# Kernel tuning notes

Hardware: AMD Instinct MI355X
Metric: run time of the kernel (lower is better)

The kernel has to match this reference:

```python
import jax, jax.numpy as jnp
import numpy as np

H = 16          # num_heads
D = 1024        # in_features
NH = D // H     # per-head dim
EPS = 1e-5


def _ln(x, g, b):
    m = jnp.mean(x, axis=-1, keepdims=True)
    v = jnp.mean((x - m) ** 2, axis=-1, keepdims=True)
    return (x - m) / jnp.sqrt(v + EPS) * g + b


def _mha(q, k, v, Wq, bq, Wk, bk, Wv, bv, causal):
    # q: [Tq,B,D], k/v: [Tk,B,D]
    Tq, B, _ = q.shape
    Tk = k.shape[0]
    qh = (q @ Wq + bq).reshape(Tq, B, H, NH)
    kh = (k @ Wk + bk).reshape(Tk, B, H, NH)
    vh = (v @ Wv + bv).reshape(Tk, B, H, NH)
    scale = 1.0 / np.float32(np.sqrt(NH))
    logits = jnp.einsum('qbhd,kbhd->bhqk', qh, kh) * scale  # [B,H,Tq,Tk]
    if causal:
        mask = jnp.tril(jnp.ones((Tq, Tk), dtype=bool))
        logits = jnp.where(mask, logits, -jnp.inf)  # softmax over prefix [0..t]
    w = jax.nn.softmax(logits, axis=-1)
    out = jnp.einsum('bhqk,kbhd->qbhd', w, vh).reshape(Tq, B, D)
    return out


def setup_inputs() -> dict:
    key = jax.random.key(0)
    ks = jax.random.split(key, 12)
    s = 0.02
    T, B = 1024, 8
    inp = {
        'encoder_input': jax.random.normal(ks[0], (T, B, D), jnp.float32),
        'decoder_input': jax.random.normal(ks[1], (T, B, D), jnp.float32),
        # self-attention projections
        'Wq1': jax.random.normal(ks[2], (D, D), jnp.float32) * s,
        'bq1': jnp.zeros((D,), jnp.float32),
        'Wk1': jax.random.normal(ks[3], (D, D), jnp.float32) * s,
        'bk1': jnp.zeros((D,), jnp.float32),
        'Wv1': jax.random.normal(ks[4], (D, D), jnp.float32) * s,
        'bv1': jnp.zeros((D,), jnp.float32),
        # cross-attention projections
        'Wq2': jax.random.normal(ks[5], (D, D), jnp.float32) * s,
        'bq2': jnp.zeros((D,), jnp.float32),
        'Wk2': jax.random.normal(ks[6], (D, D), jnp.float32) * s,
        'bk2': jnp.zeros((D,), jnp.float32),
        'Wv2': jax.random.normal(ks[7], (D, D), jnp.float32) * s,
        'bv2': jnp.zeros((D,), jnp.float32),
        # position-wise linear
        'Wl': jax.random.normal(ks[8], (D, D), jnp.float32) * s,
        'bl': jnp.zeros((D,), jnp.float32),
        # layernorms
        'g1': jnp.ones((D,), jnp.float32), 'be1': jnp.zeros((D,), jnp.float32),
        'g2': jnp.ones((D,), jnp.float32), 'be2': jnp.zeros((D,), jnp.float32),
        'g3': jnp.ones((D,), jnp.float32), 'be3': jnp.zeros((D,), jnp.float32),
    }
    return inp


def reference(encoder_input, decoder_input,
              Wq1, bq1, Wk1, bk1, Wv1, bv1,
              Wq2, bq2, Wk2, bk2, Wv2, bv2,
              Wl, bl, g1, be1, g2, be2, g3, be3):
    # causal self-attention (prefix [:t+1] per step == causal mask)
    x = _mha(decoder_input, decoder_input, decoder_input,
             Wq1, bq1, Wk1, bk1, Wv1, bv1, causal=True)
    x = _ln(x + decoder_input, g1, be1)
    # cross-attention over full encoder input
    y = _mha(x, encoder_input, encoder_input,
             Wq2, bq2, Wk2, bk2, Wv2, bv2, causal=False)
    y = _ln(y + x, g2, be2)
    # position-wise linear (no activation in source) + residual + LN
    z = y @ Wl + bl
    out = _ln(z + y, g3, be3)
    return out
```

## Files before the change

kernel.cpp:

```cpp
#include <hip/hip_runtime.h>
#include <hip/hip_bf16.h>

typedef __bf16 bf16x8 __attribute__((ext_vector_type(8)));
typedef float f32x4 __attribute__((ext_vector_type(4)));

#define MFMA16(A, B, C) __builtin_amdgcn_mfma_f32_16x16x32_bf16(A, B, C, 0, 0, 0)

#define GLDS(gp, lp)                                                              \
    __builtin_amdgcn_global_load_lds(                                             \
        (const __attribute__((address_space(1))) void*)(gp),                      \
        (__attribute__((address_space(3))) void*)(lp), 16, 0, 0)

struct PtrW { const float* p[7]; };
__global__ __launch_bounds__(256) void wt_transpose(PtrW W, __hip_bfloat16* __restrict__ Wt) {
    const float* __restrict__ src = W.p[blockIdx.z];
    __hip_bfloat16* __restrict__ dst = Wt + ((size_t)blockIdx.z << 20);
    __shared__ float tile[32][33];
    const int bn = blockIdx.x * 32;
    const int bk = blockIdx.y * 32;
    const int tx = threadIdx.x, ty = threadIdx.y;
#pragma unroll
    for (int i = 0; i < 4; i++) {
        tile[ty + i * 8][tx] = src[(size_t)(bk + ty + i * 8) * 1024 + bn + tx];
    }
    __syncthreads();
#pragma unroll
    for (int i = 0; i < 4; i++) {
        dst[(size_t)(bn + ty + i * 8) * 1024 + bk + tx] =
            __float2bfloat16(tile[tx][ty + i * 8]);
    }
}

struct PtrC { const float* s[2]; __hip_bfloat16* d[2]; };
__global__ __launch_bounds__(256) void to_bf16(PtrC c) {
    const int z = blockIdx.y;
    const int i = (blockIdx.x * 256 + threadIdx.x) * 4;
    const float4 v = *(const float4*)(c.s[z] + i);
    __align__(8) __hip_bfloat16 t[4] = {__float2bfloat16(v.x), __float2bfloat16(v.y),
                                        __float2bfloat16(v.z), __float2bfloat16(v.w)};
    *(uint2*)(c.d[z] + i) = *(const uint2*)t;
}

struct Ptr5 { const float* p[5]; };
__global__ __launch_bounds__(256) void bias_concat(Ptr5 srcs, float* __restrict__ dst) {
    const int i = threadIdx.x * 4;
    *(float4*)(dst + blockIdx.x * 1024 + i) = *(const float4*)(srcs.p[blockIdx.x] + i);
}

__global__ __launch_bounds__(256) void v_transpose(const __hip_bfloat16* __restrict__ src,
                                                   __hip_bfloat16* __restrict__ Vt,
                                                   int S, int coloff) {
    __shared__ __hip_bfloat16 tile[64][72];
    const int t0 = blockIdx.x * 64;
    const int bh = blockIdx.y;
    const int b = bh & 7, h = bh >> 3;
    const int tid = threadIdx.x;
    const int r = tid >> 2, c = (tid & 3) * 16;
    const __hip_bfloat16* sp =
        src + (size_t)((t0 + r) * 8 + b) * S + coloff + h * 64 + c;
    *(uint4*)(&tile[r][c]) = *(const uint4*)(sp);
    *(uint4*)(&tile[r][c + 8]) = *(const uint4*)(sp + 8);
    __syncthreads();
    const int d = tid >> 2, tc = (tid & 3) * 16;
    __align__(16) __hip_bfloat16 tmp[16];
#pragma unroll
    for (int j = 0; j < 16; j++) tmp[j] = tile[tc + j][d];
    __hip_bfloat16* op = Vt + ((size_t)(b * 16 + h) << 16) + (size_t)d * 1024 + t0 + tc;
    *(uint4*)(op) = *(const uint4*)(tmp);
    *(uint4*)(op + 8) = *(const uint4*)(tmp + 8);
}

__global__ __launch_bounds__(256) void gemm_bias_kernel(
    const __hip_bfloat16* __restrict__ A, const __hip_bfloat16* __restrict__ Bt,
    const float* __restrict__ bias, float* __restrict__ Cf,
    __hip_bfloat16* __restrict__ Cb, int M, int N, int K,
    float qscale, int qcols) {
    __shared__ __align__(16) __hip_bfloat16 As[2][128 * 32];
    __shared__ __align__(16) __hip_bfloat16 Bs[2][128 * 32];
    const int tid = threadIdx.x;
    const int wave = tid >> 6, lane = tid & 63;
    const int quad = lane >> 4, l16 = lane & 15;
    const int m0 = blockIdx.x * 128, n0 = blockIdx.y * 128;
    const int wm = (wave & 1) * 64, wn = (wave >> 1) * 64;
    const int srow = lane >> 2;
    const int lc = (lane & 3) ^ ((lane >> 3) & 3);
    const __hip_bfloat16* ap[2];
    const __hip_bfloat16* bp[2];
    int loff[2];
#pragma unroll
    for (int u = 0; u < 2; u++) {
        const int g = wave * 2 + u;
        const int row = g * 16 + srow;
        ap[u] = A + (size_t)(m0 + row) * K + lc * 8;
        bp[u] = Bt + (size_t)(n0 + row) * K + lc * 8;
        loff[u] = g * 512;
    }
    const int pch = quad ^ ((l16 >> 1) & 3);
    f32x4 acc[4][4] = {};
#pragma unroll
    for (int u = 0; u < 2; u++) {
        GLDS(ap[u], &As[0][loff[u]]);
        GLDS(bp[u], &Bs[0][loff[u]]);
    }
    int sel = 0;
    for (int k0 = 0; k0 < K; k0 += 32) {
        __syncthreads();
        if (k0 + 32 < K) {
#pragma unroll
            for (int u = 0; u < 2; u++) {
                GLDS(ap[u] + k0 + 32, &As[sel ^ 1][loff[u]]);
                GLDS(bp[u] + k0 + 32, &Bs[sel ^ 1][loff[u]]);
            }
        }
        bf16x8 af[4], bfr[4];
#pragma unroll
        for (int i = 0; i < 4; i++) {
            af[i] = *(const bf16x8*)(&As[sel][(wm + i * 16 + l16) * 32 + pch * 8]);
            bfr[i] = *(const bf16x8*)(&Bs[sel][(wn + i * 16 + l16) * 32 + pch * 8]);
        }
#pragma unroll
        for (int i = 0; i < 4; i++)
#pragma unroll
            for (int j = 0; j < 4; j++)
                acc[i][j] = MFMA16(af[i], bfr[j], acc[i][j]);
        sel ^= 1;
    }
#pragma unroll
    for (int i = 0; i < 4; i++) {
#pragma unroll
        for (int j = 0; j < 4; j++) {
            const int mr = m0 + wm + i * 16 + quad * 4;
            const int nc = n0 + wn + j * 16 + l16;
            const float sc = (nc < qcols) ? qscale : 1.0f;
            const float bv = bias[nc];
#pragma unroll
            for (int r = 0; r < 4; r++) {
                const float v = (acc[i][j][r] + bv) * sc;
                const size_t idx = (size_t)(mr + r) * N + nc;
                if (Cf) Cf[idx] = v;
                if (Cb) Cb[idx] = __float2bfloat16(v);
            }
        }
    }
}

__global__ __launch_bounds__(256) void attn_kernel(
    const __hip_bfloat16* __restrict__ Qp, const __hip_bfloat16* __restrict__ Kp,
    const __hip_bfloat16* __restrict__ Vt, __hip_bfloat16* __restrict__ Ob,
    int T, int qRS, int kRS, int causal) {
    __shared__ __align__(16) __hip_bfloat16 Ks[2][64 * 64];
    __shared__ __align__(16) __hip_bfloat16 Vs[2][64 * 64];
    __shared__ __align__(16) __hip_bfloat16 Ps[4][16 * 64];
    const int tid = threadIdx.x, wave = tid >> 6, lane = tid & 63;
    const int quad = lane >> 4, l16 = lane & 15;
    const int gid = blockIdx.x;
    const int bh = (gid & 7) * 16 + (gid >> 7);
    const int qt = (gid >> 3) & 15;
    const int b = bh & 7, h = bh >> 3;
    const int q0 = qt * 64;
    const int qstride = 8 * qRS, kstride = 8 * kRS;
    const int sw = l16 & 7;

    const int myq = q0 + wave * 16 + l16;
    bf16x8 qf0, qf1;
    {
        const __hip_bfloat16* qptr = Qp + (size_t)b * qRS + h * 64 + (size_t)myq * qstride;
        qf0 = *(const bf16x8*)(qptr + quad * 8);
        qf1 = *(const bf16x8*)(qptr + 32 + quad * 8);
    }
    bf16x8 onesf;
#pragma unroll
    for (int i = 0; i < 8; i++) onesf[i] = (__bf16)1.0f;

    const int jk = wave * 2;
    const int lrow = lane >> 3;
    const int lch = (lane & 7) ^ (lrow & 7);
    const __hip_bfloat16* kp0 =
        Kp + (size_t)b * kRS + h * 64 + (size_t)(jk * 8 + lrow) * kstride + lch * 8;
    const __hip_bfloat16* kp1 = kp0 + (size_t)8 * kstride;
    const __hip_bfloat16* vp0 =
        Vt + ((size_t)(b * 16 + h) << 16) + (size_t)(jk * 8 + lrow) * 1024 + lch * 8;
    const __hip_bfloat16* vp1 = vp0 + 8 * 1024;
    const size_t kinc = (size_t)64 * kstride;

    float m_i = -1e30f;
    f32x4 o[4] = {};
    f32x4 ol = {};
    const int kend = causal ? (q0 + 64) : T;
    const int qmax_w = q0 + wave * 16 + 15;

    GLDS(kp0, &Ks[0][jk * 512]);
    GLDS(kp1, &Ks[0][jk * 512 + 512]);
    GLDS(vp0, &Vs[0][jk * 512]);
    GLDS(vp1, &Vs[0][jk * 512 + 512]);
    const __hip_bfloat16* kn0 = kp0 + kinc;
    const __hip_bfloat16* kn1 = kp1 + kinc;
    const __hip_bfloat16* vn0 = vp0 + 64;
    const __hip_bfloat16* vn1 = vp1 + 64;
    int sel = 0;
    for (int k0 = 0; k0 < kend; k0 += 64) {
        __syncthreads();
        if (k0 + 64 < kend) {
            GLDS(kn0, &Ks[sel ^ 1][jk * 512]);
            GLDS(kn1, &Ks[sel ^ 1][jk * 512 + 512]);
            GLDS(vn0, &Vs[sel ^ 1][jk * 512]);
            GLDS(vn1, &Vs[sel ^ 1][jk * 512 + 512]);
            kn0 += kinc; kn1 += kinc; vn0 += 64; vn1 += 64;
        }
        if (!causal || k0 <= qmax_w) {
            f32x4 s[4];
#pragma unroll
            for (int n = 0; n < 4; n++) {
                f32x4 z = {};
                const int row = (n * 16 + l16) * 64;
                const bf16x8 kf0 = *(const bf16x8*)(&Ks[sel][row + ((quad ^ sw) << 3)]);
                const bf16x8 kf1 =
                    *(const bf16x8*)(&Ks[sel][row + (((quad + 4) ^ sw) << 3)]);
                z = MFMA16(kf0, qf0, z);
                z = MFMA16(kf1, qf1, z);
                s[n] = z;
            }
            const bool nm = causal && (k0 + 63 > q0 + wave * 16);
            float mx = -1e30f;
            if (nm) {
#pragma unroll
                for (int n = 0; n < 4; n++)
#pragma unroll
                    for (int r = 0; r < 4; r++) {
                        if (k0 + n * 16 + quad * 4 + r > myq) s[n][r] = -1e30f;
                        mx = fmaxf(mx, s[n][r]);
                    }
            } else {
#pragma unroll
                for (int n = 0; n < 4; n++)
#pragma unroll
                    for (int r = 0; r < 4; r++) mx = fmaxf(mx, s[n][r]);
            }
            mx = fmaxf(mx, __shfl_xor(mx, 16));
            mx = fmaxf(mx, __shfl_xor(mx, 32));
            const float mnew = fmaxf(m_i, mx);
            const float alpha = exp2f(m_i - mnew);
            m_i = mnew;
#pragma unroll
            for (int n = 0; n < 4; n++) {
                const float p0 = exp2f(s[n][0] - m_i);
                const float p1 = exp2f(s[n][1] - m_i);
                const float p2 = exp2f(s[n][2] - m_i);
                const float p3 = exp2f(s[n][3] - m_i);
                const __hip_bfloat162 pa = __float22bfloat162_rn(make_float2(p0, p1));
                const __hip_bfloat162 pb = __float22bfloat162_rn(make_float2(p2, p3));
                uint2 w;
                w.x = *(const unsigned int*)&pa;
                w.y = *(const unsigned int*)&pb;
                const int gcp = 2 * n + (quad >> 1);
                *(uint2*)(&Ps[wave][l16 * 64 + ((gcp ^ sw) << 3) + (quad & 1) * 4]) = w;
            }
#pragma unroll
            for (int mm = 0; mm < 4; mm++) o[mm] = o[mm] * alpha;
            ol = ol * alpha;
            const bf16x8 pf0 = *(const bf16x8*)(&Ps[wave][l16 * 64 + ((quad ^ sw) << 3)]);
            const bf16x8 pf1 =
                *(const bf16x8*)(&Ps[wave][l16 * 64 + (((quad + 4) ^ sw) << 3)]);
#pragma unroll
            for (int mm = 0; mm < 4; mm++) {
                const int vrow = (mm * 16 + l16) * 64;
                const bf16x8 vf0 = *(const bf16x8*)(&Vs[sel][vrow + ((quad ^ sw) << 3)]);
                const bf16x8 vf1 =
                    *(const bf16x8*)(&Vs[sel][vrow + (((quad + 4) ^ sw) << 3)]);
                o[mm] = MFMA16(vf0, pf0, o[mm]);
                o[mm] = MFMA16(vf1, pf1, o[mm]);
            }
            ol = MFMA16(onesf, pf0, ol);
            ol = MFMA16(onesf, pf1, ol);
        }
        sel ^= 1;
    }
    const float inv = 1.0f / ol[0];
    __hip_bfloat16* ob = Ob + (size_t)b * 1024 + h * 64 + (size_t)myq * 8192;
#pragma unroll
    for (int mm = 0; mm < 4; mm++) {
        __align__(8) __hip_bfloat16 t[4] = {
            __float2bfloat16(o[mm][0] * inv), __float2bfloat16(o[mm][1] * inv),
            __float2bfloat16(o[mm][2] * inv), __float2bfloat16(o[mm][3] * inv)};
        *(uint2*)(ob + mm * 16 + quad * 4) = *(const uint2*)t;
    }
}

__global__ __launch_bounds__(256) void ln_res_kernel(
    const __hip_bfloat16* __restrict__ a, const float* __restrict__ bres,
    const float* __restrict__ g, const float* __restrict__ be,
    float* __restrict__ outf, __hip_bfloat16* __restrict__ outb) {
    const int row = blockIdx.x;
    const int tid = threadIdx.x;
    const size_t off = (size_t)row * 1024 + tid * 4;
    uint2 ar = *(const uint2*)(a + off);
    const __hip_bfloat16* ah = (const __hip_bfloat16*)&ar;
    const float4 vb = *(const float4*)(bres + off);
    float x0 = __bfloat162float(ah[0]) + vb.x;
    float x1 = __bfloat162float(ah[1]) + vb.y;
    float x2 = __bfloat162float(ah[2]) + vb.z;
    float x3 = __bfloat162float(ah[3]) + vb.w;
    float s = x0 + x1 + x2 + x3;
    float ss = x0 * x0 + x1 * x1 + x2 * x2 + x3 * x3;
#pragma unroll
    for (int w = 32; w >= 1; w >>= 1) {
        s += __shfl_xor(s, w);
        ss += __shfl_xor(ss, w);
    }
    __shared__ float sm[4], sv[4];
    const int wave = tid >> 6;
    if ((tid & 63) == 0) { sm[wave] = s; sv[wave] = ss; }
    __syncthreads();
    s = sm[0] + sm[1] + sm[2] + sm[3];
    ss = sv[0] + sv[1] + sv[2] + sv[3];
    const float mean = s * (1.f / 1024.f);
    const float inv = rsqrtf(ss * (1.f / 1024.f) - mean * mean + 1e-5f);
    const float4 gg = *(const float4*)(g + tid * 4);
    const float4 bb = *(const float4*)(be + tid * 4);
    const float y0 = (x0 - mean) * inv * gg.x + bb.x;
    const float y1 = (x1 - mean) * inv * gg.y + bb.y;
    const float y2 = (x2 - mean) * inv * gg.z + bb.z;
    const float y3 = (x3 - mean) * inv * gg.w + bb.w;
    if (outf) *(float4*)(outf + off) = make_float4(y0, y1, y2, y3);
    if (outb) {
        __align__(8) __hip_bfloat16 t[4] = {__float2bfloat16(y0), __float2bfloat16(y1),
                                            __float2bfloat16(y2), __float2bfloat16(y3)};
        *(uint2*)(outb + off) = *(const uint2*)t;
    }
}

extern "C" void kernel_launch(void* const* d_in, const int* in_sizes, int n_in,
                              void* d_out, int out_size, void* d_ws, size_t ws_size,
                              hipStream_t stream) {
    const float* enc = (const float*)d_in[0];
    const float* dec = (const float*)d_in[1];
    const float* Wq1 = (const float*)d_in[2];
    const float* bq1 = (const float*)d_in[3];
    const float* Wk1 = (const float*)d_in[4];
    const float* bk1 = (const float*)d_in[5];
    const float* Wv1 = (const float*)d_in[6];
    const float* bv1 = (const float*)d_in[7];
    const float* Wq2 = (const float*)d_in[8];
    const float* bq2 = (const float*)d_in[9];
    const float* Wk2 = (const float*)d_in[10];
    const float* bk2 = (const float*)d_in[11];
    const float* Wv2 = (const float*)d_in[12];
    const float* bv2 = (const float*)d_in[13];
    const float* Wl = (const float*)d_in[14];
    const float* bl = (const float*)d_in[15];
    const float* g1 = (const float*)d_in[16];
    const float* be1 = (const float*)d_in[17];
    const float* g2 = (const float*)d_in[18];
    const float* be2 = (const float*)d_in[19];
    const float* g3 = (const float*)d_in[20];
    const float* be3 = (const float*)d_in[21];
    float* outp = (float*)d_out;

    char* p = (char*)d_ws;
    auto alloc = [&](size_t n) {
        char* r = p;
        p += (n + 255) & ~(size_t)255;
        return r;
    };
    const size_t MD = (size_t)8192 * 1024;
    __hip_bfloat16* enc_b = (__hip_bfloat16*)alloc(MD * 2);
    __hip_bfloat16* dec_b = (__hip_bfloat16*)alloc(MD * 2);
    __hip_bfloat16* Wt = (__hip_bfloat16*)alloc((size_t)7 * 1024 * 1024 * 2);
    float* bcat = (float*)alloc((3072 + 2048) * sizeof(float));
    __hip_bfloat16* qkv = (__hip_bfloat16*)alloc(MD * 3 * 2);
    __hip_bfloat16* qb = (__hip_bfloat16*)alloc(MD * 2);
    __hip_bfloat16* attnb = (__hip_bfloat16*)alloc(MD * 2);
    __hip_bfloat16* Vtb = (__hip_bfloat16*)alloc(MD * 2);
    float* xf = (float*)alloc(MD * 4);
    float* yf = (float*)alloc(MD * 4);
    __hip_bfloat16* xb = dec_b;
    __hip_bfloat16* yb = enc_b;

    const float QSC = 0.18033688f;

    PtrW wptrs = {{Wq1, Wk1, Wv1, Wq2, Wk2, Wv2, Wl}};
    wt_transpose<<<dim3(32, 32, 7), dim3(32, 8), 0, stream>>>(wptrs, Wt);
    PtrC cp = {{enc, dec}, {enc_b, dec_b}};
    to_bf16<<<dim3(8192, 2), 256, 0, stream>>>(cp);
    Ptr5 bp = {{bq1, bk1, bv1, bk2, bv2}};
    bias_concat<<<5, 256, 0, stream>>>(bp, bcat);

    gemm_bias_kernel<<<dim3(64, 24), 256, 0, stream>>>(dec_b, Wt, bcat, nullptr, qkv,
                                                       8192, 3072, 1024, QSC, 1024);
    v_transpose<<<dim3(16, 128), 256, 0, stream>>>(qkv, Vtb, 3072, 2048);
    attn_kernel<<<2048, 256, 0, stream>>>(qkv, qkv + 1024, Vtb, attnb,
                                          1024, 3072, 3072, 1);
    ln_res_kernel<<<8192, 256, 0, stream>>>(attnb, dec, g1, be1, xf, xb);

    gemm_bias_kernel<<<dim3(64, 8), 256, 0, stream>>>(
        xb, Wt + (size_t)3 * 1024 * 1024, bq2, nullptr, qb, 8192, 1024, 1024, QSC, 1024);
    gemm_bias_kernel<<<dim3(64, 16), 256, 0, stream>>>(
        enc_b, Wt + (size_t)4 * 1024 * 1024, bcat + 3072, nullptr, qkv, 8192, 2048, 1024,
        1.0f, 0);
    v_transpose<<<dim3(16, 128), 256, 0, stream>>>(qkv, Vtb, 2048, 1024);
    attn_kernel<<<2048, 256, 0, stream>>>(qb, qkv, Vtb, attnb, 1024, 1024, 2048, 0);
    ln_res_kernel<<<8192, 256, 0, stream>>>(attnb, xf, g2, be2, yf, yb);

    gemm_bias_kernel<<<dim3(64, 8), 256, 0, stream>>>(
        yb, Wt + (size_t)6 * 1024 * 1024, bl, nullptr, qb, 8192, 1024, 1024, 1.0f, 0);
    ln_res_kernel<<<8192, 256, 0, stream>>>(qb, yf, g3, be3, outp, nullptr);
}
```

Before: 543.3 us.

## Process two query tiles per wave and load K/V directly from global

Reworks the attention kernel so each block handles 128 queries, with each wave owning two 16-row query groups that share the same K and V fragments. The LDS double-buffered K/V staging through global_load_lds is replaced by direct per-lane global loads into registers, and exp2f is swapped for the hardware exp2 builtin. The grid is halved accordingly. This aims to cut K/V traffic per query and remove block-wide barriers. The cost is higher register pressure, uncoalesced strided global K loads with no prefetch, and worse causal load balance because each block now covers larger query tiles.

```diff
diff --git a/kernel.cpp b/kernel.cpp
--- a/kernel.cpp
+++ b/kernel.cpp
@@ -148,141 +148,137 @@
     const __hip_bfloat16* __restrict__ Qp, const __hip_bfloat16* __restrict__ Kp,
     const __hip_bfloat16* __restrict__ Vt, __hip_bfloat16* __restrict__ Ob,
     int T, int qRS, int kRS, int causal) {
-    __shared__ __align__(16) __hip_bfloat16 Ks[2][64 * 64];
-    __shared__ __align__(16) __hip_bfloat16 Vs[2][64 * 64];
     __shared__ __align__(16) __hip_bfloat16 Ps[4][16 * 64];
     const int tid = threadIdx.x, wave = tid >> 6, lane = tid & 63;
     const int quad = lane >> 4, l16 = lane & 15;
     const int gid = blockIdx.x;
-    const int bh = (gid & 7) * 16 + (gid >> 7);
-    const int qt = (gid >> 3) & 15;
+    const int bh = (gid & 7) * 16 + ((gid >> 3) & 15);
+    const int qt = gid >> 7;
     const int b = bh & 7, h = bh >> 3;
-    const int q0 = qt * 64;
+    const int q0 = qt * 128;
     const int qstride = 8 * qRS, kstride = 8 * kRS;
     const int sw = l16 & 7;
 
-    const int myq = q0 + wave * 16 + l16;
-    bf16x8 qf0, qf1;
-    {
-        const __hip_bfloat16* qptr = Qp + (size_t)b * qRS + h * 64 + (size_t)myq * qstride;
-        qf0 = *(const bf16x8*)(qptr + quad * 8);
-        qf1 = *(const bf16x8*)(qptr + 32 + quad * 8);
-    }
+    const int qg0 = q0 + wave * 16;
+    const int qg1 = q0 + 64 + wave * 16;
+    const int myq0 = qg0 + l16, myq1 = qg1 + l16;
+    const __hip_bfloat16* qbase = Qp + (size_t)b * qRS + h * 64;
+    const bf16x8 qf00 = *(const bf16x8*)(qbase + (size_t)myq0 * qstride + quad * 8);
+    const bf16x8 qf01 = *(const bf16x8*)(qbase + (size_t)myq0 * qstride + 32 + quad * 8);
+    const bf16x8 qf10 = *(const bf16x8*)(qbase + (size_t)myq1 * qstride + quad * 8);
+    const bf16x8 qf11 = *(const bf16x8*)(qbase + (size_t)myq1 * qstride + 32 + quad * 8);
     bf16x8 onesf;
 #pragma unroll
     for (int i = 0; i < 8; i++) onesf[i] = (__bf16)1.0f;
 
-    const int jk = wave * 2;
-    const int lrow = lane >> 3;
-    const int lch = (lane & 7) ^ (lrow & 7);
-    const __hip_bfloat16* kp0 =
-        Kp + (size_t)b * kRS + h * 64 + (size_t)(jk * 8 + lrow) * kstride + lch * 8;
-    const __hip_bfloat16* kp1 = kp0 + (size_t)8 * kstride;
-    const __hip_bfloat16* vp0 =
-        Vt + ((size_t)(b * 16 + h) << 16) + (size_t)(jk * 8 + lrow) * 1024 + lch * 8;
-    const __hip_bfloat16* vp1 = vp0 + 8 * 1024;
-    const size_t kinc = (size_t)64 * kstride;
-
-    float m_i = -1e30f;
-    f32x4 o[4] = {};
-    f32x4 ol = {};
-    const int kend = causal ? (q0 + 64) : T;
-    const int qmax_w = q0 + wave * 16 + 15;
-
-    GLDS(kp0, &Ks[0][jk * 512]);
-    GLDS(kp1, &Ks[0][jk * 512 + 512]);
-    GLDS(vp0, &Vs[0][jk * 512]);
-    GLDS(vp1, &Vs[0][jk * 512 + 512]);
-    const __hip_bfloat16* kn0 = kp0 + kinc;
-    const __hip_bfloat16* kn1 = kp1 + kinc;
-    const __hip_bfloat16* vn0 = vp0 + 64;
-    const __hip_bfloat16* vn1 = vp1 + 64;
-    int sel = 0;
+    const __hip_bfloat16* kb = Kp + (size_t)b * kRS + h * 64;
+    const __hip_bfloat16* vbp = Vt + ((size_t)(b * 16 + h) << 16);
+
+    float m0 = -1e30f, m1 = -1e30f;
+    f32x4 o0[4] = {}, o1[4] = {};
+    f32x4 ol0 = {}, ol1 = {};
+    bf16x8 pf00, pf01, pf10, pf11;
+
+    auto softmax = [&](f32x4* s, float& m_i, f32x4* o, f32x4& ol, int qg, int myq,
+                       bf16x8& pf0, bf16x8& pf1, int k0) {
+        const bool nm = causal && (k0 + 63 > qg);
+        float mx = -1e30f;
+        if (nm) {
+#pragma unroll
+            for (int n = 0; n < 4; n++)
+#pragma unroll
+                for (int r = 0; r < 4; r++) {
+                    if (k0 + n * 16 + quad * 4 + r > myq) s[n][r] = -1e30f;
+                    mx = fmaxf(mx, s[n][r]);
+                }
+        } else {
+#pragma unroll
+            for (int n = 0; n < 4; n++)
+#pragma unroll
+                for (int r = 0; r < 4; r++) mx = fmaxf(mx, s[n][r]);
+        }
+        mx = fmaxf(mx, __shfl_xor(mx, 16));
+        mx = fmaxf(mx, __shfl_xor(mx, 32));
+        const float mnew = fmaxf(m_i, mx);
+        const float alpha = __builtin_amdgcn_exp2f(m_i - mnew);
+        m_i = mnew;
+#pragma unroll
+        for (int n = 0; n < 4; n++) {
+            const float p0 = __builtin_amdgcn_exp2f(s[n][0] - m_i);
+            const float p1 = __builtin_amdgcn_exp2f(s[n][1] - m_i);
+            const float p2 = __builtin_amdgcn_exp2f(s[n][2] - m_i);
+            const float p3 = __builtin_amdgcn_exp2f(s[n][3] - m_i);
+            const __hip_bfloat162 pa = __float22bfloat162_rn(make_float2(p0, p1));
+            const __hip_bfloat162 pb = __float22bfloat162_rn(make_float2(p2, p3));
+            uint2 w;
+            w.x = *(const unsigned int*)&pa;
+            w.y = *(const unsigned int*)&pb;
+            const int gcp = 2 * n + (quad >> 1);
+            *(uint2*)(&Ps[wave][l16 * 64 + ((gcp ^ sw) << 3) + (quad & 1) * 4]) = w;
+        }
+#pragma unroll
+        for (int mm = 0; mm < 4; mm++) o[mm] = o[mm] * alpha;
+        ol = ol * alpha;
+        pf0 = *(const bf16x8*)(&Ps[wave][l16 * 64 + ((quad ^ sw) << 3)]);
+        pf1 = *(const bf16x8*)(&Ps[wave][l16 * 64 + (((quad + 4) ^ sw) << 3)]);
+        ol = MFMA16(onesf, pf0, ol);
+        ol = MFMA16(onesf, pf1, ol);
+    };
+
+    const int kend = causal ? (q0 + 128) : T;
     for (int k0 = 0; k0 < kend; k0 += 64) {
-        __syncthreads();
-        if (k0 + 64 < kend) {
-            GLDS(kn0, &Ks[sel ^ 1][jk * 512]);
-            GLDS(kn1, &Ks[sel ^ 1][jk * 512 + 512]);
-            GLDS(vn0, &Vs[sel ^ 1][jk * 512]);
-            GLDS(vn1, &Vs[sel ^ 1][jk * 512 + 512]);
-            kn0 += kinc; kn1 += kinc; vn0 += 64; vn1 += 64;
-        }
-        if (!causal || k0 <= qmax_w) {
-            f32x4 s[4];
+        const bool act0 = !causal || (k0 <= qg0 + 15);
+        f32x4 s0[4] = {}, s1[4] = {};
+        {
+            bf16x8 kf[4];
+#pragma unroll
+            for (int n = 0; n < 4; n++)
+                kf[n] = *(const bf16x8*)(kb + (size_t)(k0 + n * 16 + l16) * kstride +
+                                         quad * 8);
 #pragma unroll
             for (int n = 0; n < 4; n++) {
-                f32x4 z = {};
-                const int row = (n * 16 + l16) * 64;
-                const bf16x8 kf0 = *(const bf16x8*)(&Ks[sel][row + ((quad ^ sw) << 3)]);
-                const bf16x8 kf1 =
-                    *(const bf16x8*)(&Ks[sel][row + (((quad + 4) ^ sw) << 3)]);
-                z = MFMA16(kf0, qf0, z);
-                z = MFMA16(kf1, qf1, z);
-                s[n] = z;
+                if (act0) s0[n] = MFMA16(kf[n], qf00, s0[n]);
+                s1[n] = MFMA16(kf[n], qf10, s1[n]);
             }
-            const bool nm = causal && (k0 + 63 > q0 + wave * 16);
-            float mx = -1e30f;
-            if (nm) {
-#pragma unroll
-                for (int n = 0; n < 4; n++)
-#pragma unroll
-                    for (int r = 0; r < 4; r++) {
-                        if (k0 + n * 16 + quad * 4 + r > myq) s[n][r] = -1e30f;
-                        mx = fmaxf(mx, s[n][r]);
-                    }
-            } else {
-#pragma unroll
-                for (int n = 0; n < 4; n++)
-#pragma unroll
-                    for (int r = 0; r < 4; r++) mx = fmaxf(mx, s[n][r]);
+#pragma unroll
+            for (int n = 0; n < 4; n++)
+                kf[n] = *(const bf16x8*)(kb + (size_t)(k0 + n * 16 + l16) * kstride + 32 +
+                                         quad * 8);
+#pragma unroll
+            for (int n = 0; n < 4; n++) {
+                if (act0) s0[n] = MFMA16(kf[n], qf01, s0[n]);
+                s1[n] = MFMA16(kf[n], qf11, s1[n]);
             }
-            mx = fmaxf(mx, __shfl_xor(mx, 16));
-            mx = fmaxf(mx, __shfl_xor(mx, 32));
-            const float mnew = fmaxf(m_i, mx);
-            const float alpha = exp2f(m_i - mnew);
-            m_i = mnew;
-#pragma unroll
-            for (int n = 0; n < 4; n++) {
-                const float p0 = exp2f(s[n][0] - m_i);
-                const float p1 = exp2f(s[n][1] - m_i);
-                const float p2 = exp2f(s[n][2] - m_i);
-                const float p3 = exp2f(s[n][3] - m_i);
-                const __hip_bfloat162 pa = __float22bfloat162_rn(make_float2(p0, p1));
-                const __hip_bfloat162 pb = __float22bfloat162_rn(make_float2(p2, p3));
-                uint2 w;
-                w.x = *(const unsigned int*)&pa;
-                w.y = *(const unsigned int*)&pb;
-                const int gcp = 2 * n + (quad >> 1);
-                *(uint2*)(&Ps[wave][l16 * 64 + ((gcp ^ sw) << 3) + (quad & 1) * 4]) = w;
+        }
+        if (act0) softmax(s0, m0, o0, ol0, qg0, myq0, pf00, pf01, k0);
+        softmax(s1, m1, o1, ol1, qg1, myq1, pf10, pf11, k0);
+#pragma unroll
+        for (int mm = 0; mm < 4; mm++) {
+            const __hip_bfloat16* vr = vbp + (size_t)(mm * 16 + l16) * 1024 + k0;
+            const bf16x8 vf0 = *(const bf16x8*)(vr + quad * 8);
+            const bf16x8 vf1 = *(const bf16x8*)(vr + 32 + quad * 8);
+            if (act0) {
+                o0[mm] = MFMA16(vf0, pf00, o0[mm]);
+                o0[mm] = MFMA16(vf1, pf01, o0[mm]);
             }
-#pragma unroll
-            for (int mm = 0; mm < 4; mm++) o[mm] = o[mm] * alpha;
-            ol = ol * alpha;
-            const bf16x8 pf0 = *(const bf16x8*)(&Ps[wave][l16 * 64 + ((quad ^ sw) << 3)]);
-            const bf16x8 pf1 =
-                *(const bf16x8*)(&Ps[wave][l16 * 64 + (((quad + 4) ^ sw) << 3)]);
-#pragma unroll
-            for (int mm = 0; mm < 4; mm++) {
-                const int vrow = (mm * 16 + l16) * 64;
-                const bf16x8 vf0 = *(const bf16x8*)(&Vs[sel][vrow + ((quad ^ sw) << 3)]);
-                const bf16x8 vf1 =
-                    *(const bf16x8*)(&Vs[sel][vrow + (((quad + 4) ^ sw) << 3)]);
-                o[mm] = MFMA16(vf0, pf0, o[mm]);
-                o[mm] = MFMA16(vf1, pf1, o[mm]);
-            }
-            ol = MFMA16(onesf, pf0, ol);
-            ol = MFMA16(onesf, pf1, ol);
-        }
-        sel ^= 1;
-    }
-    const float inv = 1.0f / ol[0];
-    __hip_bfloat16* ob = Ob + (size_t)b * 1024 + h * 64 + (size_t)myq * 8192;
+            o1[mm] = MFMA16(vf0, pf10, o1[mm]);
+            o1[mm] = MFMA16(vf1, pf11, o1[mm]);
+        }
+    }
+    const float inv0 = 1.0f / ol0[0];
+    const float inv1 = 1.0f / ol1[0];
+    __hip_bfloat16* ob0 = Ob + (size_t)b * 1024 + h * 64 + (size_t)myq0 * 8192;
+    __hip_bfloat16* ob1 = Ob + (size_t)b * 1024 + h * 64 + (size_t)myq1 * 8192;
 #pragma unroll
     for (int mm = 0; mm < 4; mm++) {
-        __align__(8) __hip_bfloat16 t[4] = {
-            __float2bfloat16(o[mm][0] * inv), __float2bfloat16(o[mm][1] * inv),
-            __float2bfloat16(o[mm][2] * inv), __float2bfloat16(o[mm][3] * inv)};
-        *(uint2*)(ob + mm * 16 + quad * 4) = *(const uint2*)t;
+        __align__(8) __hip_bfloat16 t0[4] = {
+            __float2bfloat16(o0[mm][0] * inv0), __float2bfloat16(o0[mm][1] * inv0),
+            __float2bfloat16(o0[mm][2] * inv0), __float2bfloat16(o0[mm][3] * inv0)};
+        *(uint2*)(ob0 + mm * 16 + quad * 4) = *(const uint2*)t0;
+        __align__(8) __hip_bfloat16 t1[4] = {
+            __float2bfloat16(o1[mm][0] * inv1), __float2bfloat16(o1[mm][1] * inv1),
+            __float2bfloat16(o1[mm][2] * inv1), __float2bfloat16(o1[mm][3] * inv1)};
+        *(uint2*)(ob1 + mm * 16 + quad * 4) = *(const uint2*)t1;
     }
 }
 
@@ -388,7 +384,7 @@
     gemm_bias_kernel<<<dim3(64, 24), 256, 0, stream>>>(dec_b, Wt, bcat, nullptr, qkv,
                                                        8192, 3072, 1024, QSC, 1024);
     v_transpose<<<dim3(16, 128), 256, 0, stream>>>(qkv, Vtb, 3072, 2048);
-    attn_kernel<<<2048, 256, 0, stream>>>(qkv, qkv + 1024, Vtb, attnb,
+    attn_kernel<<<1024, 256, 0, stream>>>(qkv, qkv + 1024, Vtb, attnb,
                                           1024, 3072, 3072, 1);
     ln_res_kernel<<<8192, 256, 0, stream>>>(attnb, dec, g1, be1, xf, xb);
 
@@ -398,7 +394,7 @@
         enc_b, Wt + (size_t)4 * 1024 * 1024, bcat + 3072, nullptr, qkv, 8192, 2048, 1024,
         1.0f, 0);
     v_transpose<<<dim3(16, 128), 256, 0, stream>>>(qkv, Vtb, 2048, 1024);
-    attn_kernel<<<2048, 256, 0, stream>>>(qb, qkv, Vtb, attnb, 1024, 1024, 2048, 0);
+    attn_kernel<<<1024, 256, 0, stream>>>(qb, qkv, Vtb, attnb, 1024, 1024, 2048, 0);
     ln_res_kernel<<<8192, 256, 0, stream>>>(attnb, xf, g2, be2, yf, yb);
 
     gemm_bias_kernel<<<dim3(64, 8), 256, 0, stream>>>(
```

New measurement: 613.5 us. 12.9% more time.
